# Performance work log

Measured on AMD Instinct MI355X. Metric: run time of the kernel, lower is better.

Reference implementation:

```python
import jax, jax.numpy as jnp
import numpy as np

D_MODEL = 1024
NHEAD = 16
HEAD_DIM = D_MODEL // NHEAD
MASK_FILLER = -1e20


def setup_inputs() -> dict:
    key = jax.random.key(0)
    ks = jax.random.split(key, 8)
    B, S = 2, 2048
    query = jax.random.normal(ks[0], (B, S, D_MODEL), dtype=jnp.float32)
    key_t = jax.random.normal(ks[1], (B, S, D_MODEL), dtype=jnp.float32)
    value = jax.random.normal(ks[2], (B, S, D_MODEL), dtype=jnp.float32)
    mask = jax.random.randint(ks[3], (B, S, S), 0, 2, dtype=jnp.int32)
    # nn.Linear(d_model, d_model, bias=False) weights, shape [out, in]
    scale = 1.0 / np.sqrt(D_MODEL)
    wq = jax.random.uniform(ks[4], (D_MODEL, D_MODEL), jnp.float32, -scale, scale)
    wk = jax.random.uniform(ks[5], (D_MODEL, D_MODEL), jnp.float32, -scale, scale)
    wv = jax.random.uniform(ks[6], (D_MODEL, D_MODEL), jnp.float32, -scale, scale)
    wo = jax.random.uniform(ks[7], (D_MODEL, D_MODEL), jnp.float32, -scale, scale)
    return {"query": query, "key": key_t, "value": value, "mask": mask,
            "wq": wq, "wk": wk, "wv": wv, "wo": wo}


def reference(query, key, value, mask, wq, wk, wv, wo):
    B = query.shape[0]
    # Projections: nn.Linear -> x @ W.T
    q = (query @ wq.T).reshape(B, -1, NHEAD, HEAD_DIM).transpose(0, 2, 1, 3)  # [B,H,Sq,Dh]
    k = (key @ wk.T).reshape(B, -1, NHEAD, HEAD_DIM).transpose(0, 2, 1, 3)    # [B,H,Sk,Dh]
    v = (value @ wv.T).reshape(B, -1, NHEAD, HEAD_DIM).transpose(0, 2, 1, 3)  # [B,H,Sk,Dh]
    scores = jnp.einsum('bhqd,bhkd->bhqk', q, k) / jnp.sqrt(jnp.float32(HEAD_DIM))
    scores = jnp.where(mask[:, None, :, :] == 0, MASK_FILLER, scores)
    attn = jax.nn.softmax(scores, axis=-1)  # dropout p=0.0 -> identity
    out = jnp.einsum('bhqk,bhkd->bhqd', attn, v)  # [B,H,Sq,Dh]
    out = out.transpose(0, 2, 1, 3).reshape(B, -1, D_MODEL)
    return out @ wo.T
```

## Files before the change

kernel.cpp:

```cpp
#include <hip/hip_runtime.h>
#include <stdint.h>

typedef __bf16 bf16x8 __attribute__((ext_vector_type(8)));
typedef float floatx4 __attribute__((ext_vector_type(4)));
typedef unsigned short ushort8v __attribute__((ext_vector_type(8)));
typedef unsigned int uint4v __attribute__((ext_vector_type(4)));
typedef unsigned short u16;
typedef unsigned long long u64;

#define GLOAD_LDS16(gp, lp)                                                       \
  __builtin_amdgcn_global_load_lds((__attribute__((address_space(1))) void*)(gp), \
                                   (__attribute__((address_space(3))) void*)(lp), \
                                   16, 0, 0)

__device__ __forceinline__ u16 f2bf(float f) {
  uint32_t u = __builtin_bit_cast(uint32_t, f);
  u = (u + 0x7FFFu + ((u >> 16) & 1u)) >> 16;
  return (u16)u;
}
__device__ __forceinline__ u16 f2bf_up(float f) {
  return (u16)((__builtin_bit_cast(uint32_t, f) + 0x8000u) >> 16);
}

__device__ __forceinline__ ushort8v load8(const void* base, size_t elemOff, int isf32) {
  if (isf32) {
    const uint32_t* p = (const uint32_t*)base + elemOff;
    uint4v a = *(const uint4v*)p;
    uint4v b = *(const uint4v*)(p + 4);
#pragma unroll
    for (int i = 0; i < 4; ++i) { a[i] += 0x8000u; b[i] += 0x8000u; }
    uint4v r;
    r[0] = __builtin_amdgcn_perm(a[1], a[0], 0x07060302);
    r[1] = __builtin_amdgcn_perm(a[3], a[2], 0x07060302);
    r[2] = __builtin_amdgcn_perm(b[1], b[0], 0x07060302);
    r[3] = __builtin_amdgcn_perm(b[3], b[2], 0x07060302);
    return __builtin_bit_cast(ushort8v, r);
  }
  return *(const ushort8v*)((const u16*)base + elemOff);
}

__global__ void detect_dtype(const u16* __restrict__ q, int* __restrict__ flag) {
  if (threadIdx.x == 0) *flag = 0;
  __syncthreads();
  int hit = 0;
  for (int i = threadIdx.x; i < 8192; i += 256) {
    u16 u = q[i];
    if (((u >> 7) & 0xFF) == 0xFF) hit = 1;
  }
  if (hit) atomicOr(flag, 1);
}

__global__ void pack_mask(const int* __restrict__ mask, u64* __restrict__ mpk) {
  const int gw   = (blockIdx.x * 256 + threadIdx.x) >> 6;
  const int lane = threadIdx.x & 63;
  const int word = gw & 31;
  const int row  = gw >> 5;
  const int m = mask[(size_t)row * 2048 + word * 64 + lane];
  u64 bits = __ballot(m != 0);
  if (lane == 0) mpk[(size_t)row * 32 + word] = bits;
}

__global__ __launch_bounds__(256)
void cvt_all(const void* X0, const void* X1, const void* X2,
             const void* W0, const void* W1, const void* W2, const void* W3,
             u16* __restrict__ Xb, u16* __restrict__ Wb, const int* flagp)
{
  const int isf = *flagp;
  const int id = blockIdx.x;
  const int t  = threadIdx.x;
  const int r2  = t >> 7;
  const int col = (t & 127) * 8;
  const void* src; u16* dst; int row;
  if (id < 6144) {
    const int s = id >> 11;
    src = (s == 0) ? X0 : (s == 1) ? X1 : X2;
    row = (id & 2047) * 2 + r2;
    dst = Xb + (size_t)s * 4096 * 1040 + (size_t)row * 1040 + col;
  } else {
    const int s = (id - 6144) >> 9;
    src = (s == 0) ? W0 : (s == 1) ? W1 : (s == 2) ? W2 : W3;
    row = ((id - 6144) & 511) * 2 + r2;
    dst = Wb + (size_t)s * 1024 * 1040 + (size_t)row * 1040 + col;
  }
  *(ushort8v*)dst = load8(src, (size_t)row * 1024 + col, isf);
}

__global__ __launch_bounds__(256)
void cvt_w(const void* W0, const void* W1, const void* W2, const void* W3,
           u16* __restrict__ dst, const int* flagp) {
  const int isf = *flagp;
  const int z = blockIdx.y;
  const void* src = (z == 0) ? W0 : (z == 1) ? W1 : (z == 2) ? W2 : W3;
  const size_t off = ((size_t)blockIdx.x * 256 + threadIdx.x) * 8;
  *(ushort8v*)(dst + (size_t)z * 1024 * 1024 + off) = load8(src, off, isf);
}

__global__ __launch_bounds__(256, 3)
void gemm_qkv_b(const u16* __restrict__ Xb, const u16* __restrict__ Wb,
                u16* __restrict__ Qb, u16* __restrict__ Kb, u16* __restrict__ Vt)
{
  const int AS = 1040, WS = 1040, N = 1024, K = 1024;
  const int z = blockIdx.z;
  const u16* A = Xb + (size_t)z * 4096 * AS;
  const u16* W = Wb + (size_t)z * 1024 * WS;

  __shared__ __align__(16) u16 lA[2 * 128 * 32];
  __shared__ __align__(16) u16 lB[2 * 128 * 32];

  const int tid  = threadIdx.x;
  const int lane = tid & 63;
  const int quad = lane >> 4;
  const int l15  = lane & 15;
  const int w    = tid >> 6;
  const int wm   = w >> 1, wn = w & 1;
  const int tileM = blockIdx.x * 128;
  const int tileN = blockIdx.y * 128;

  floatx4 acc[4][4] = {};

  const int ldRow = tid >> 2;
  const int ldCol = (tid & 3) * 8;
  const u16* aG = A + (size_t)(tileM + ldRow) * AS + ldCol;
  const u16* bG = W + (size_t)(tileN + ldRow) * WS + ldCol;
  u16* lAp = lA + tid * 8;
  u16* lBp = lB + tid * 8;

  GLOAD_LDS16(aG, lAp);
  GLOAD_LDS16(aG + (size_t)64 * AS, lAp + 2048);
  GLOAD_LDS16(bG, lBp);
  GLOAD_LDS16(bG + (size_t)64 * WS, lBp + 2048);
  __syncthreads();

#pragma unroll 2
  for (int k0 = 0; k0 < K; k0 += 32) {
    const int cur = (k0 >> 5) & 1;
    const int nxo = 4096 * (cur ^ 1);
    if (k0 + 32 < K) {
      GLOAD_LDS16(aG + k0 + 32, lAp + nxo);
      GLOAD_LDS16(aG + (size_t)64 * AS + k0 + 32, lAp + nxo + 2048);
      GLOAD_LDS16(bG + k0 + 32, lBp + nxo);
      GLOAD_LDS16(bG + (size_t)64 * WS + k0 + 32, lBp + nxo + 2048);
    }
    const u16* cA = lA + 4096 * cur;
    const u16* cB = lB + 4096 * cur;
    bf16x8 af[4], bw[4];
#pragma unroll
    for (int i = 0; i < 4; ++i) {
      af[i] = *(const bf16x8*)&cA[(wm * 64 + i * 16 + l15) * 32 + quad * 8];
      bw[i] = *(const bf16x8*)&cB[(wn * 64 + i * 16 + l15) * 32 + quad * 8];
    }
#pragma unroll
    for (int i = 0; i < 4; ++i)
#pragma unroll
      for (int j = 0; j < 4; ++j)
        acc[i][j] = __builtin_amdgcn_mfma_f32_16x16x32_bf16(af[i], bw[j], acc[i][j], 0, 0, 0);
    __syncthreads();
  }

  if (z < 2) {
    u16* C = (z == 0) ? Qb : Kb;
    const float sc = (z == 0) ? 0.125f : 1.0f;
#pragma unroll
    for (int i = 0; i < 4; ++i) {
      const int row0 = tileM + wm * 64 + i * 16 + quad * 4;
#pragma unroll
      for (int j = 0; j < 4; ++j) {
        const int col = tileN + wn * 64 + j * 16 + l15;
#pragma unroll
        for (int r = 0; r < 4; ++r)
          C[(size_t)(row0 + r) * N + col] = f2bf(acc[i][j][r] * sc);
      }
    }
  } else {
    const int half = w >> 1;
    u16* myT = (w & 1) ? lB : lA;
#pragma unroll
    for (int pass = 0; pass < 2; ++pass) {
      __syncthreads();
      if (half == pass) {
#pragma unroll
        for (int i = 0; i < 4; ++i)
#pragma unroll
          for (int j = 0; j < 4; ++j)
#pragma unroll
            for (int r = 0; r < 4; ++r) {
              const int lr = i * 16 + quad * 4 + r;
              const int lc = j * 16 + l15;
              myT[lr * 64 + (lc ^ (quad << 4))] = f2bf(acc[i][j][r]);
            }
      }
      __syncthreads();
      if (half == pass) {
        const int n    = lane;
        const int gcol = tileN + wn * 64 + n;
        const int hh = gcol >> 6, dd = gcol & 63;
        const int growBase = tileM + wm * 64;
        const int bb = growBase >> 11;
        const int s0 = growBase & 2047;
        u16* dst = Vt + (((size_t)bb * 16 + hh) * 64 + dd) * 2048 + s0;
#pragma unroll
        for (int m0 = 0; m0 < 64; m0 += 8) {
          ushort8v pk;
#pragma unroll
          for (int t = 0; t < 8; ++t) {
            const int m = m0 + t;
            pk[t] = myT[m * 64 + (n ^ ((m & 12) << 2))];
          }
          *(ushort8v*)(dst + m0) = pk;
        }
      }
    }
  }
}

__global__ __launch_bounds__(256)
void gemm_qkv_f(const void* X0, const void* X1, const void* X2,
                const u16* __restrict__ Wb,
                u16* __restrict__ Qb, u16* __restrict__ Kb, u16* __restrict__ Vt,
                const int* flagp)
{
  const int K = 1024, N = 1024;
  const int isf = *flagp;
  const int z = blockIdx.z;
  const void* A_ = (z == 0) ? X0 : (z == 1) ? X1 : X2;
  const u16* W = Wb + (size_t)z * 1024 * 1024;

  __shared__ __align__(16) u16 lA[128 * 32];
  __shared__ __align__(16) u16 lB[128 * 32];

  const int tid  = threadIdx.x;
  const int lane = tid & 63;
  const int quad = lane >> 4;
  const int l15  = lane & 15;
  const int w    = tid >> 6;
  const int wm   = w >> 1, wn = w & 1;
  const int tileM = blockIdx.x * 128;
  const int tileN = blockIdx.y * 128;

  floatx4 acc[4][4] = {};

  const int ldRow = tid >> 2;
  const int ldCol = (tid & 3) * 8;
  const size_t aOff = (size_t)(tileM + ldRow) * K + ldCol;
  const u16* bG = W + (size_t)(tileN + ldRow) * K + ldCol;
  u16* lAp = lA + tid * 8;
  u16* lBp = lB + tid * 8;

  ushort8v a0 = load8(A_, aOff, isf);
  ushort8v a1 = load8(A_, aOff + (size_t)64 * K, isf);
  ushort8v b0 = *(const ushort8v*)bG;
  ushort8v b1 = *(const ushort8v*)(bG + (size_t)64 * K);

  for (int k0 = 0; k0 < K; k0 += 32) {
    __syncthreads();
    *(ushort8v*)lAp          = a0;
    *(ushort8v*)(lAp + 2048) = a1;
    *(ushort8v*)lBp          = b0;
    *(ushort8v*)(lBp + 2048) = b1;
    __syncthreads();

    if (k0 + 32 < K) {
      a0 = load8(A_, aOff + k0 + 32, isf);
      a1 = load8(A_, aOff + (size_t)64 * K + k0 + 32, isf);
      b0 = *(const ushort8v*)(bG + k0 + 32);
      b1 = *(const ushort8v*)(bG + (size_t)64 * K + k0 + 32);
    }

    bf16x8 af[4], bw[4];
#pragma unroll
    for (int i = 0; i < 4; ++i) {
      af[i] = *(const bf16x8*)&lA[(wm * 64 + i * 16 + l15) * 32 + quad * 8];
      bw[i] = *(const bf16x8*)&lB[(wn * 64 + i * 16 + l15) * 32 + quad * 8];
    }
#pragma unroll
    for (int i = 0; i < 4; ++i)
#pragma unroll
      for (int j = 0; j < 4; ++j)
        acc[i][j] = __builtin_amdgcn_mfma_f32_16x16x32_bf16(af[i], bw[j], acc[i][j], 0, 0, 0);
  }

  if (z < 2) {
    u16* C = (z == 0) ? Qb : Kb;
    const float sc = (z == 0) ? 0.125f : 1.0f;
#pragma unroll
    for (int i = 0; i < 4; ++i) {
      const int row0 = tileM + wm * 64 + i * 16 + quad * 4;
#pragma unroll
      for (int j = 0; j < 4; ++j) {
        const int col = tileN + wn * 64 + j * 16 + l15;
#pragma unroll
        for (int r = 0; r < 4; ++r)
          C[(size_t)(row0 + r) * N + col] = f2bf(acc[i][j][r] * sc);
      }
    }
  } else {
    const int half = w >> 1;
    u16* myT = (w & 1) ? lB : lA;
#pragma unroll
    for (int pass = 0; pass < 2; ++pass) {
      __syncthreads();
      if (half == pass) {
#pragma unroll
        for (int i = 0; i < 4; ++i)
#pragma unroll
          for (int j = 0; j < 4; ++j)
#pragma unroll
            for (int r = 0; r < 4; ++r) {
              const int lr = i * 16 + quad * 4 + r;
              const int lc = j * 16 + l15;
              myT[lr * 64 + (lc ^ (quad << 4))] = f2bf(acc[i][j][r]);
            }
      }
      __syncthreads();
      if (half == pass) {
        const int n    = lane;
        const int gcol = tileN + wn * 64 + n;
        const int hh = gcol >> 6, dd = gcol & 63;
        const int growBase = tileM + wm * 64;
        const int bb = growBase >> 11;
        const int s0 = growBase & 2047;
        u16* dst = Vt + (((size_t)bb * 16 + hh) * 64 + dd) * 2048 + s0;
#pragma unroll
        for (int m0 = 0; m0 < 64; m0 += 8) {
          ushort8v pk;
#pragma unroll
          for (int t = 0; t < 8; ++t) {
            const int m = m0 + t;
            pk[t] = myT[m * 64 + (n ^ ((m & 12) << 2))];
          }
          *(ushort8v*)(dst + m0) = pk;
        }
      }
    }
  }
}

__global__ __launch_bounds__(256)
void attn(const u16* Qb, const u16* __restrict__ Kb, const u16* __restrict__ Vt,
          const u64* __restrict__ mpk, u16* AO, int aoStr)
{
  __shared__ __align__(16) u16 lK[64 * 72];
  __shared__ __align__(16) u16 lV[64 * 72];
  __shared__ __align__(16) u16 lP[64 * 72];

  const int tid  = threadIdx.x;
  const int lane = tid & 63;
  const int quad = lane >> 4;
  const int l15  = lane & 15;
  const int w    = tid >> 6;

  const int bh = blockIdx.x;
  const int qt = blockIdx.y;
  const int b  = bh >> 4;
  const int h  = bh & 15;
  const size_t rowB   = (size_t)b * 2048;
  const size_t vtBase = ((size_t)bh * 64) * 2048;

  bf16x8 aq[2];
  {
    const u16* qp = Qb + (rowB + qt * 64 + w * 16 + l15) * 1024 + h * 64 + quad * 8;
    aq[0] = *(const bf16x8*)qp;
    aq[1] = *(const bf16x8*)(qp + 32);
  }

  const ushort8v one_u = {0x3F80, 0x3F80, 0x3F80, 0x3F80, 0x3F80, 0x3F80, 0x3F80, 0x3F80};
  const bf16x8 ones = __builtin_bit_cast(bf16x8, one_u);

  floatx4 o[4], l4;
#pragma unroll
  for (int nb = 0; nb < 4; ++nb) o[nb] = (floatx4){0.f, 0.f, 0.f, 0.f};
  l4 = (floatx4){0.f, 0.f, 0.f, 0.f};

  const int qrow0 = qt * 64 + w * 16 + quad * 4;
  const u64* mrow = mpk + (rowB + qrow0) * 32;
  u16* lPw = lP + (w * 16) * 72;

  const int sr = tid >> 3;
  const int sc = (tid & 7) * 8;
  const u16* kG = Kb + (rowB + sr) * 1024 + h * 64 + sc;
  const u16* vG = Vt + vtBase + (size_t)sr * 2048 + sc;

  ushort8v k0 = *(const ushort8v*)kG;
  ushort8v k1 = *(const ushort8v*)(kG + (size_t)32 * 1024);
  ushort8v v0 = *(const ushort8v*)vG;
  ushort8v v1 = *(const ushort8v*)(vG + (size_t)32 * 2048);

  for (int kt = 0; kt < 32; ++kt) {
    __syncthreads();
    *(ushort8v*)(lK + sr * 72 + sc)        = k0;
    *(ushort8v*)(lK + (sr + 32) * 72 + sc) = k1;
    *(ushort8v*)(lV + sr * 72 + sc)        = v0;
    *(ushort8v*)(lV + (sr + 32) * 72 + sc) = v1;
    __syncthreads();

    if (kt < 31) {
      const u16* gk = kG + (size_t)((kt + 1) * 64) * 1024;
      k0 = *(const ushort8v*)gk;
      k1 = *(const ushort8v*)(gk + (size_t)32 * 1024);
      const u16* gv = vG + (kt + 1) * 64;
      v0 = *(const ushort8v*)gv;
      v1 = *(const ushort8v*)(gv + (size_t)32 * 2048);
    }

    u64 mw[4];
#pragma unroll
    for (int r = 0; r < 4; ++r) mw[r] = mrow[(size_t)r * 32 + kt];

#pragma unroll
    for (int nb = 0; nb < 4; ++nb) {
      const u16* kp = &lK[(nb * 16 + l15) * 72 + quad * 8];
      bf16x8 bk0 = *(const bf16x8*)kp;
      bf16x8 bk1 = *(const bf16x8*)(kp + 32);
      floatx4 sacc = {0.f, 0.f, 0.f, 0.f};
      sacc = __builtin_amdgcn_mfma_f32_16x16x32_bf16(aq[0], bk0, sacc, 0, 0, 0);
      sacc = __builtin_amdgcn_mfma_f32_16x16x32_bf16(aq[1], bk1, sacc, 0, 0, 0);
      const int kbit = nb * 16 + l15;
#pragma unroll
      for (int r = 0; r < 4; ++r) {
        const float s = ((mw[r] >> kbit) & 1ULL) ? sacc[r] : -1e20f;
        lPw[(quad * 4 + r) * 72 + nb * 16 + l15] = f2bf_up(__expf(s));
      }
    }

#pragma unroll
    for (int ks = 0; ks < 2; ++ks) {
      bf16x8 ap = *(const bf16x8*)&lPw[l15 * 72 + ks * 32 + quad * 8];
#pragma unroll
      for (int nb = 0; nb < 4; ++nb) {
        bf16x8 bv = *(const bf16x8*)&lV[(nb * 16 + l15) * 72 + ks * 32 + quad * 8];
        o[nb] = __builtin_amdgcn_mfma_f32_16x16x32_bf16(ap, bv, o[nb], 0, 0, 0);
      }
      l4 = __builtin_amdgcn_mfma_f32_16x16x32_bf16(ap, ones, l4, 0, 0, 0);
    }
  }

#pragma unroll
  for (int r = 0; r < 4; ++r) {
    const float inv = 1.0f / l4[r];
    const size_t orow = (rowB + qt * 64 + w * 16 + quad * 4 + r) * aoStr + h * 64;
#pragma unroll
    for (int nb = 0; nb < 4; ++nb)
      AO[orow + nb * 16 + l15] = f2bf(o[nb][r] * inv);
  }
}

__global__ __launch_bounds__(256, 3)
void gemm_out(const u16* __restrict__ A, int aStr,
              const u16* __restrict__ W, int wStr, void* C_, const int* flagp)
{
  const int K = 1024, N = 1024;
  const int isf = *flagp;

  __shared__ __align__(16) u16 lA[2 * 64 * 32];
  __shared__ __align__(16) u16 lB[2 * 128 * 32];

  const int tid  = threadIdx.x;
  const int lane = tid & 63;
  const int quad = lane >> 4;
  const int l15  = lane & 15;
  const int w    = tid >> 6;
  const int tileM = blockIdx.x * 64;
  const int tileN = blockIdx.y * 128;

  floatx4 acc[4][2] = {};

  const int ldRow = tid >> 2;
  const int ldCol = (tid & 3) * 8;
  const u16* aG = A + (size_t)(tileM + ldRow) * aStr + ldCol;
  const u16* bG = W + (size_t)(tileN + ldRow) * wStr + ldCol;
  u16* lAp = lA + tid * 8;
  u16* lBp = lB + tid * 8;

  GLOAD_LDS16(aG, lAp);
  GLOAD_LDS16(bG, lBp);
  GLOAD_LDS16(bG + (size_t)64 * wStr, lBp + 2048);
  __syncthreads();

#pragma unroll 2
  for (int k0 = 0; k0 < K; k0 += 32) {
    const int cur = (k0 >> 5) & 1;
    const int nxA = 2048 * (cur ^ 1);
    const int nxB = 4096 * (cur ^ 1);
    if (k0 + 32 < K) {
      GLOAD_LDS16(aG + k0 + 32, lAp + nxA);
      GLOAD_LDS16(bG + k0 + 32, lBp + nxB);
      GLOAD_LDS16(bG + (size_t)64 * wStr + k0 + 32, lBp + nxB + 2048);
    }
    const u16* cA = lA + 2048 * cur;
    const u16* cB = lB + 4096 * cur;
    bf16x8 af[4], bw[2];
#pragma unroll
    for (int i = 0; i < 4; ++i)
      af[i] = *(const bf16x8*)&cA[(i * 16 + l15) * 32 + quad * 8];
#pragma unroll
    for (int j = 0; j < 2; ++j)
      bw[j] = *(const bf16x8*)&cB[(w * 32 + j * 16 + l15) * 32 + quad * 8];
#pragma unroll
    for (int i = 0; i < 4; ++i)
#pragma unroll
      for (int j = 0; j < 2; ++j)
        acc[i][j] = __builtin_amdgcn_mfma_f32_16x16x32_bf16(af[i], bw[j], acc[i][j], 0, 0, 0);
    __syncthreads();
  }

#pragma unroll
  for (int i = 0; i < 4; ++i) {
    const int row0 = tileM + i * 16 + quad * 4;
#pragma unroll
    for (int j = 0; j < 2; ++j) {
      const int col = tileN + w * 32 + j * 16 + l15;
#pragma unroll
      for (int r = 0; r < 4; ++r) {
        const size_t off = (size_t)(row0 + r) * N + col;
        if (isf) ((float*)C_)[off] = acc[i][j][r];
        else     ((u16*)C_)[off]   = f2bf(acc[i][j][r]);
      }
    }
  }
}

extern "C" void kernel_launch(void* const* d_in, const int* in_sizes, int n_in,
                              void* d_out, int out_size, void* d_ws, size_t ws_size,
                              hipStream_t stream)
{
  const int* mk = (const int*)d_in[3];

  int* flag = (int*)d_ws;
  u64* mpk  = (u64*)((char*)d_ws + 256);
  const size_t SZ = (size_t)4096 * 1024;
  u16* Qb = (u16*)((char*)d_ws + 256 + (size_t)1048576);
  u16* Kb = Qb + SZ;
  u16* Vt = Kb + SZ;
  u16* Wb = Vt + SZ;

  const size_t WB_PAD = (size_t)4 * 1024 * 1040;
  const size_t XB_PAD = (size_t)3 * 4096 * 1040;
  const size_t NEED = 256 + 1048576 + 3 * SZ * 2 + WB_PAD * 2 + XB_PAD * 2;

  detect_dtype<<<1, 256, 0, stream>>>((const u16*)d_in[0], flag);
  pack_mask<<<32768, 256, 0, stream>>>(mk, mpk);

  if (ws_size >= NEED) {
    u16* Xb = Wb + WB_PAD;
    cvt_all<<<8192, 256, 0, stream>>>(d_in[0], d_in[1], d_in[2],
                                      d_in[4], d_in[5], d_in[6], d_in[7],
                                      Xb, Wb, flag);
    gemm_qkv_b<<<dim3(32, 8, 3), 256, 0, stream>>>(Xb, Wb, Qb, Kb, Vt);
    u16* AOp = Xb;
    attn<<<dim3(32, 32), 256, 0, stream>>>(Qb, Kb, Vt, mpk, AOp, 1040);
    gemm_out<<<dim3(64, 8), 256, 0, stream>>>(AOp, 1040,
                                              Wb + (size_t)3 * 1024 * 1040, 1040,
                                              d_out, flag);
  } else {
    cvt_w<<<dim3(512, 4), 256, 0, stream>>>(d_in[4], d_in[5], d_in[6], d_in[7], Wb, flag);
    gemm_qkv_f<<<dim3(32, 8, 3), 256, 0, stream>>>(d_in[0], d_in[1], d_in[2],
                                                   Wb, Qb, Kb, Vt, flag);
    attn<<<dim3(32, 32), 256, 0, stream>>>(Qb, Kb, Vt, mpk, Qb, 1024);
    gemm_out<<<dim3(64, 8), 256, 0, stream>>>(Qb, 1024,
                                              Wb + (size_t)3 * 1024 * 1024, 1024,
                                              d_out, flag);
  }
}
```

Before: 297.1 us.

## Double-buffer attention K/V via direct global-to-LDS loads with XOR swizzle

```diff
diff --git a/kernel.cpp b/kernel.cpp
--- a/kernel.cpp
+++ b/kernel.cpp
@@ -159,7 +159,7 @@
 
   if (z < 2) {
     u16* C = (z == 0) ? Qb : Kb;
-    const float sc = (z == 0) ? 0.125f : 1.0f;
+    const float sc = (z == 0) ? 0.18033688011112042f : 1.0f;
 #pragma unroll
     for (int i = 0; i < 4; ++i) {
       const int row0 = tileM + wm * 64 + i * 16 + quad * 4;
@@ -281,7 +281,7 @@
 
   if (z < 2) {
     u16* C = (z == 0) ? Qb : Kb;
-    const float sc = (z == 0) ? 0.125f : 1.0f;
+    const float sc = (z == 0) ? 0.18033688011112042f : 1.0f;
 #pragma unroll
     for (int i = 0; i < 4; ++i) {
       const int row0 = tileM + wm * 64 + i * 16 + quad * 4;
@@ -339,9 +339,9 @@
 void attn(const u16* Qb, const u16* __restrict__ Kb, const u16* __restrict__ Vt,
           const u64* __restrict__ mpk, u16* AO, int aoStr)
 {
-  __shared__ __align__(16) u16 lK[64 * 72];
-  __shared__ __align__(16) u16 lV[64 * 72];
-  __shared__ __align__(16) u16 lP[64 * 72];
+  __shared__ __align__(16) u16 lK[2][64 * 64];
+  __shared__ __align__(16) u16 lV[2][64 * 64];
+  __shared__ __align__(16) u16 lP[64 * 64];
 
   const int tid  = threadIdx.x;
   const int lane = tid & 63;
@@ -373,33 +373,29 @@
 
   const int qrow0 = qt * 64 + w * 16 + quad * 4;
   const u64* mrow = mpk + (rowB + qrow0) * 32;
-  u16* lPw = lP + (w * 16) * 72;
-
-  const int sr = tid >> 3;
-  const int sc = (tid & 7) * 8;
-  const u16* kG = Kb + (rowB + sr) * 1024 + h * 64 + sc;
-  const u16* vG = Vt + vtBase + (size_t)sr * 2048 + sc;
-
-  ushort8v k0 = *(const ushort8v*)kG;
-  ushort8v k1 = *(const ushort8v*)(kG + (size_t)32 * 1024);
-  ushort8v v0 = *(const ushort8v*)vG;
-  ushort8v v1 = *(const ushort8v*)(vG + (size_t)32 * 2048);
-
+  u16* lPw = lP + w * 1024;
+
+  const int r1 = tid >> 3;
+  const int cs = ((tid & 7) ^ (r1 & 7)) * 8;
+  const u16* kSrc = Kb + (rowB + r1) * 1024 + h * 64 + cs;
+  const u16* vSrc = Vt + vtBase + (size_t)r1 * 2048 + cs;
+
+  GLOAD_LDS16(kSrc,                     &lK[0][tid * 8]);
+  GLOAD_LDS16(kSrc + (size_t)32 * 1024, &lK[0][tid * 8 + 2048]);
+  GLOAD_LDS16(vSrc,                     &lV[0][tid * 8]);
+  GLOAD_LDS16(vSrc + (size_t)32 * 2048, &lV[0][tid * 8 + 2048]);
+  __syncthreads();
+
+#pragma unroll 2
   for (int kt = 0; kt < 32; ++kt) {
-    __syncthreads();
-    *(ushort8v*)(lK + sr * 72 + sc)        = k0;
-    *(ushort8v*)(lK + (sr + 32) * 72 + sc) = k1;
-    *(ushort8v*)(lV + sr * 72 + sc)        = v0;
-    *(ushort8v*)(lV + (sr + 32) * 72 + sc) = v1;
-    __syncthreads();
-
+    const int cur = kt & 1;
     if (kt < 31) {
-      const u16* gk = kG + (size_t)((kt + 1) * 64) * 1024;
-      k0 = *(const ushort8v*)gk;
-      k1 = *(const ushort8v*)(gk + (size_t)32 * 1024);
-      const u16* gv = vG + (kt + 1) * 64;
-      v0 = *(const ushort8v*)gv;
-      v1 = *(const ushort8v*)(gv + (size_t)32 * 2048);
+      const u16* kS = kSrc + (size_t)(kt + 1) * 64 * 1024;
+      const u16* vS = vSrc + (kt + 1) * 64;
+      GLOAD_LDS16(kS,                     &lK[cur ^ 1][tid * 8]);
+      GLOAD_LDS16(kS + (size_t)32 * 1024, &lK[cur ^ 1][tid * 8 + 2048]);
+      GLOAD_LDS16(vS,                     &lV[cur ^ 1][tid * 8]);
+      GLOAD_LDS16(vS + (size_t)32 * 2048, &lV[cur ^ 1][tid * 8 + 2048]);
     }
 
     u64 mw[4];
@@ -408,30 +404,35 @@
 
 #pragma unroll
     for (int nb = 0; nb < 4; ++nb) {
-      const u16* kp = &lK[(nb * 16 + l15) * 72 + quad * 8];
-      bf16x8 bk0 = *(const bf16x8*)kp;
-      bf16x8 bk1 = *(const bf16x8*)(kp + 32);
+      const int row = nb * 16 + l15;
+      const int swk = (row & 7) << 3;
+      bf16x8 bk0 = *(const bf16x8*)&lK[cur][row * 64 + ((quad * 8) ^ swk)];
+      bf16x8 bk1 = *(const bf16x8*)&lK[cur][row * 64 + ((quad * 8 + 32) ^ swk)];
       floatx4 sacc = {0.f, 0.f, 0.f, 0.f};
       sacc = __builtin_amdgcn_mfma_f32_16x16x32_bf16(aq[0], bk0, sacc, 0, 0, 0);
       sacc = __builtin_amdgcn_mfma_f32_16x16x32_bf16(aq[1], bk1, sacc, 0, 0, 0);
       const int kbit = nb * 16 + l15;
 #pragma unroll
       for (int r = 0; r < 4; ++r) {
-        const float s = ((mw[r] >> kbit) & 1ULL) ? sacc[r] : -1e20f;
-        lPw[(quad * 4 + r) * 72 + nb * 16 + l15] = f2bf_up(__expf(s));
+        const float e = __builtin_amdgcn_exp2f(sacc[r]);
+        const float p = ((mw[r] >> kbit) & 1ULL) ? e : 0.0f;
+        const int prow = quad * 4 + r;
+        lPw[prow * 64 + (kbit ^ ((prow >> 1) << 3))] = f2bf_up(p);
       }
     }
 
 #pragma unroll
     for (int ks = 0; ks < 2; ++ks) {
-      bf16x8 ap = *(const bf16x8*)&lPw[l15 * 72 + ks * 32 + quad * 8];
+      bf16x8 ap = *(const bf16x8*)&lPw[l15 * 64 + ((ks * 32 + quad * 8) ^ ((l15 >> 1) << 3))];
 #pragma unroll
       for (int nb = 0; nb < 4; ++nb) {
-        bf16x8 bv = *(const bf16x8*)&lV[(nb * 16 + l15) * 72 + ks * 32 + quad * 8];
+        const int row = nb * 16 + l15;
+        bf16x8 bv = *(const bf16x8*)&lV[cur][row * 64 + ((ks * 32 + quad * 8) ^ ((row & 7) << 3))];
         o[nb] = __builtin_amdgcn_mfma_f32_16x16x32_bf16(ap, bv, o[nb], 0, 0, 0);
       }
       l4 = __builtin_amdgcn_mfma_f32_16x16x32_bf16(ap, ones, l4, 0, 0, 0);
     }
+    __syncthreads();
   }
 
 #pragma unroll
```

Result: faster. 287.7 us (-3.2%).
